# Optimization experiments

Hardware: AMD Instinct MI355X
Metric: run time of the kernel (lower is better)

The kernel has to match this reference:

```python
import jax, jax.numpy as jnp
import numpy as np

EPS = 1e-6


def setup_inputs() -> dict:
    key = jax.random.key(0)
    k1, k2, k3 = jax.random.split(key, 3)
    B, S, HC = 32, 16384, 4
    mixes = jax.random.normal(k1, (B, S, 2 * HC + HC * HC), dtype=jnp.float32)
    hc_scale = jax.random.uniform(k2, (3,), dtype=jnp.float32)
    hc_base = jax.random.normal(k3, (2 * HC + HC * HC,), dtype=jnp.float32)
    return {"mixes": mixes, "hc_scale": hc_scale, "hc_base": hc_base,
            "hc_mult": HC, "sinkhorn_iters": 20}


def reference(mixes, hc_scale, hc_base, hc_mult, sinkhorn_iters):
    hm = hc_mult
    pre = mixes[..., :hm]                       # [B,S,hm]
    post = mixes[..., hm:2 * hm]                # [B,S,hm]
    comb = mixes[..., 2 * hm:]                  # [B,S,hm*hm]
    comb = comb.reshape(comb.shape[:-1] + (hm, hm))  # [B,S,hm,hm]

    pre = jax.nn.sigmoid(pre * hc_scale[0] + hc_base[:hm]) + EPS
    post = 2.0 * jax.nn.sigmoid(post * hc_scale[1] + hc_base[hm:2 * hm])
    comb = comb * hc_scale[2] + hc_base[2 * hm:].reshape(hm, hm)
    comb = jax.nn.softmax(comb, axis=-1) + EPS

    # Sinkhorn normalization: alternate column / row normalization.
    comb = comb / (comb.sum(axis=-2, keepdims=True) + EPS)
    for _ in range(sinkhorn_iters - 1):
        comb = comb / (comb.sum(axis=-1, keepdims=True) + EPS)
        comb = comb / (comb.sum(axis=-2, keepdims=True) + EPS)
    return pre, post, comb
```

## Files before the change

### kernel.cpp

```cpp
#include <hip/hip_runtime.h>


constexpr float EPSF  = 1e-6f;
constexpr float LOG2E = 1.4426950408889634f;

__device__ __forceinline__ float frcp(float x) { return __builtin_amdgcn_rcpf(x); }
__device__ __forceinline__ float fexp(float x) { return __builtin_amdgcn_exp2f(x * LOG2E); }

__global__ __launch_bounds__(256) void hc_sinkhorn_kernel(
    const float* __restrict__ mixes,
    const float* __restrict__ hc_scale,
    const float* __restrict__ hc_base,
    float* __restrict__ out_pre,
    float* __restrict__ out_post,
    float* __restrict__ out_comb,
    int nrows)
{
    const int r = blockIdx.x * blockDim.x + threadIdx.x;
    if (r >= nrows) return;

    const float s0 = hc_scale[0];
    const float s1 = hc_scale[1];
    const float s2 = hc_scale[2];

    const float4* src = reinterpret_cast<const float4*>(mixes) + (size_t)r * 6;
    const float4 vpre  = src[0];
    const float4 vpost = src[1];
    const float4 c0    = src[2];
    const float4 c1    = src[3];
    const float4 c2    = src[4];
    const float4 c3    = src[5];

    float pre[4]  = {vpre.x,  vpre.y,  vpre.z,  vpre.w};
    float post[4] = {vpost.x, vpost.y, vpost.z, vpost.w};
    #pragma unroll
    for (int i = 0; i < 4; ++i) {
        pre[i]  = frcp(1.0f + fexp(-(pre[i]  * s0 + hc_base[i]))) + EPSF;
        post[i] = 2.0f * frcp(1.0f + fexp(-(post[i] * s1 + hc_base[4 + i])));
    }

    float c[4][4];
    c[0][0] = c0.x * s2 + hc_base[ 8]; c[0][1] = c0.y * s2 + hc_base[ 9];
    c[0][2] = c0.z * s2 + hc_base[10]; c[0][3] = c0.w * s2 + hc_base[11];
    c[1][0] = c1.x * s2 + hc_base[12]; c[1][1] = c1.y * s2 + hc_base[13];
    c[1][2] = c1.z * s2 + hc_base[14]; c[1][3] = c1.w * s2 + hc_base[15];
    c[2][0] = c2.x * s2 + hc_base[16]; c[2][1] = c2.y * s2 + hc_base[17];
    c[2][2] = c2.z * s2 + hc_base[18]; c[2][3] = c2.w * s2 + hc_base[19];
    c[3][0] = c3.x * s2 + hc_base[20]; c[3][1] = c3.y * s2 + hc_base[21];
    c[3][2] = c3.z * s2 + hc_base[22]; c[3][3] = c3.w * s2 + hc_base[23];

    #pragma unroll
    for (int i = 0; i < 4; ++i) {
        const float m  = fmaxf(fmaxf(c[i][0], c[i][1]), fmaxf(c[i][2], c[i][3]));
        const float e0 = fexp(c[i][0] - m);
        const float e1 = fexp(c[i][1] - m);
        const float e2 = fexp(c[i][2] - m);
        const float e3 = fexp(c[i][3] - m);
        const float rs = frcp(e0 + e1 + e2 + e3);
        c[i][0] = e0 * rs + EPSF;
        c[i][1] = e1 * rs + EPSF;
        c[i][2] = e2 * rs + EPSF;
        c[i][3] = e3 * rs + EPSF;
    }

    #pragma unroll
    for (int j = 0; j < 4; ++j) {
        const float s  = c[0][j] + c[1][j] + c[2][j] + c[3][j];
        const float rs = frcp(s + EPSF);
        c[0][j] *= rs; c[1][j] *= rs; c[2][j] *= rs; c[3][j] *= rs;
    }
    for (int it = 0; it < 19; ++it) {
        #pragma unroll
        for (int i = 0; i < 4; ++i) {
            const float s  = c[i][0] + c[i][1] + c[i][2] + c[i][3];
            const float rs = frcp(s + EPSF);
            c[i][0] *= rs; c[i][1] *= rs; c[i][2] *= rs; c[i][3] *= rs;
        }
        #pragma unroll
        for (int j = 0; j < 4; ++j) {
            const float s  = c[0][j] + c[1][j] + c[2][j] + c[3][j];
            const float rs = frcp(s + EPSF);
            c[0][j] *= rs; c[1][j] *= rs; c[2][j] *= rs; c[3][j] *= rs;
        }
    }

    reinterpret_cast<float4*>(out_pre)[r]  = make_float4(pre[0],  pre[1],  pre[2],  pre[3]);
    reinterpret_cast<float4*>(out_post)[r] = make_float4(post[0], post[1], post[2], post[3]);
    float4* oc = reinterpret_cast<float4*>(out_comb) + (size_t)r * 4;
    oc[0] = make_float4(c[0][0], c[0][1], c[0][2], c[0][3]);
    oc[1] = make_float4(c[1][0], c[1][1], c[1][2], c[1][3]);
    oc[2] = make_float4(c[2][0], c[2][1], c[2][2], c[2][3]);
    oc[3] = make_float4(c[3][0], c[3][1], c[3][2], c[3][3]);
}

extern "C" void kernel_launch(void* const* d_in, const int* in_sizes, int n_in,
                              void* d_out, int out_size, void* d_ws, size_t ws_size,
                              hipStream_t stream) {
    const float* mixes    = (const float*)d_in[0];
    const float* hc_scale = (const float*)d_in[1];
    const float* hc_base  = (const float*)d_in[2];

    const int nrows = in_sizes[0] / 24;
    float* out      = (float*)d_out;
    float* out_pre  = out;
    float* out_post = out + (size_t)nrows * 4;
    float* out_comb = out + (size_t)nrows * 8;

    const int block = 256;
    const int grid  = (nrows + block - 1) / block;
    hc_sinkhorn_kernel<<<grid, block, 0, stream>>>(
        mixes, hc_scale, hc_base, out_pre, out_post, out_comb, nrows);
}
```

Baseline: 113.4 us.

## Stage row loads and comb stores through padded LDS for coalesced access

```diff
diff --git a/kernel.cpp b/kernel.cpp
--- a/kernel.cpp
+++ b/kernel.cpp
@@ -4,50 +4,29 @@
 constexpr float EPSF  = 1e-6f;
 constexpr float LOG2E = 1.4426950408889634f;
 
+constexpr int RPB        = 256;
+constexpr int IN_STRIDE  = 25;
+constexpr int OUT_STRIDE = 17;
+
 __device__ __forceinline__ float frcp(float x) { return __builtin_amdgcn_rcpf(x); }
 __device__ __forceinline__ float fexp(float x) { return __builtin_amdgcn_exp2f(x * LOG2E); }
 
-__global__ __launch_bounds__(256) void hc_sinkhorn_kernel(
-    const float* __restrict__ mixes,
-    const float* __restrict__ hc_scale,
-    const float* __restrict__ hc_base,
-    float* __restrict__ out_pre,
-    float* __restrict__ out_post,
-    float* __restrict__ out_comb,
-    int nrows)
+__device__ __forceinline__ void compute_row(
+    const float row[24], const float base[24],
+    float s0, float s1, float s2,
+    float pre[4], float post[4], float c[4][4])
 {
-    const int r = blockIdx.x * blockDim.x + threadIdx.x;
-    if (r >= nrows) return;
-
-    const float s0 = hc_scale[0];
-    const float s1 = hc_scale[1];
-    const float s2 = hc_scale[2];
-
-    const float4* src = reinterpret_cast<const float4*>(mixes) + (size_t)r * 6;
-    const float4 vpre  = src[0];
-    const float4 vpost = src[1];
-    const float4 c0    = src[2];
-    const float4 c1    = src[3];
-    const float4 c2    = src[4];
-    const float4 c3    = src[5];
-
-    float pre[4]  = {vpre.x,  vpre.y,  vpre.z,  vpre.w};
-    float post[4] = {vpost.x, vpost.y, vpost.z, vpost.w};
     #pragma unroll
     for (int i = 0; i < 4; ++i) {
-        pre[i]  = frcp(1.0f + fexp(-(pre[i]  * s0 + hc_base[i]))) + EPSF;
-        post[i] = 2.0f * frcp(1.0f + fexp(-(post[i] * s1 + hc_base[4 + i])));
+        pre[i]  = frcp(1.0f + fexp(-(row[i]     * s0 + base[i])))     + EPSF;
+        post[i] = 2.0f * frcp(1.0f + fexp(-(row[4 + i] * s1 + base[4 + i])));
     }
 
-    float c[4][4];
-    c[0][0] = c0.x * s2 + hc_base[ 8]; c[0][1] = c0.y * s2 + hc_base[ 9];
-    c[0][2] = c0.z * s2 + hc_base[10]; c[0][3] = c0.w * s2 + hc_base[11];
-    c[1][0] = c1.x * s2 + hc_base[12]; c[1][1] = c1.y * s2 + hc_base[13];
-    c[1][2] = c1.z * s2 + hc_base[14]; c[1][3] = c1.w * s2 + hc_base[15];
-    c[2][0] = c2.x * s2 + hc_base[16]; c[2][1] = c2.y * s2 + hc_base[17];
-    c[2][2] = c2.z * s2 + hc_base[18]; c[2][3] = c2.w * s2 + hc_base[19];
-    c[3][0] = c3.x * s2 + hc_base[20]; c[3][1] = c3.y * s2 + hc_base[21];
-    c[3][2] = c3.z * s2 + hc_base[22]; c[3][3] = c3.w * s2 + hc_base[23];
+    #pragma unroll
+    for (int i = 0; i < 4; ++i)
+        #pragma unroll
+        for (int j = 0; j < 4; ++j)
+            c[i][j] = row[8 + 4 * i + j] * s2 + base[8 + 4 * i + j];
 
     #pragma unroll
     for (int i = 0; i < 4; ++i) {
@@ -65,32 +44,106 @@
 
     #pragma unroll
     for (int j = 0; j < 4; ++j) {
-        const float s  = c[0][j] + c[1][j] + c[2][j] + c[3][j];
-        const float rs = frcp(s + EPSF);
+        const float rs = frcp(c[0][j] + c[1][j] + c[2][j] + c[3][j] + EPSF);
         c[0][j] *= rs; c[1][j] *= rs; c[2][j] *= rs; c[3][j] *= rs;
     }
     for (int it = 0; it < 19; ++it) {
         #pragma unroll
         for (int i = 0; i < 4; ++i) {
-            const float s  = c[i][0] + c[i][1] + c[i][2] + c[i][3];
-            const float rs = frcp(s + EPSF);
+            const float rs = frcp(c[i][0] + c[i][1] + c[i][2] + c[i][3] + EPSF);
             c[i][0] *= rs; c[i][1] *= rs; c[i][2] *= rs; c[i][3] *= rs;
         }
         #pragma unroll
         for (int j = 0; j < 4; ++j) {
-            const float s  = c[0][j] + c[1][j] + c[2][j] + c[3][j];
-            const float rs = frcp(s + EPSF);
+            const float rs = frcp(c[0][j] + c[1][j] + c[2][j] + c[3][j] + EPSF);
             c[0][j] *= rs; c[1][j] *= rs; c[2][j] *= rs; c[3][j] *= rs;
         }
     }
+}
 
-    reinterpret_cast<float4*>(out_pre)[r]  = make_float4(pre[0],  pre[1],  pre[2],  pre[3]);
-    reinterpret_cast<float4*>(out_post)[r] = make_float4(post[0], post[1], post[2], post[3]);
-    float4* oc = reinterpret_cast<float4*>(out_comb) + (size_t)r * 4;
-    oc[0] = make_float4(c[0][0], c[0][1], c[0][2], c[0][3]);
-    oc[1] = make_float4(c[1][0], c[1][1], c[1][2], c[1][3]);
-    oc[2] = make_float4(c[2][0], c[2][1], c[2][2], c[2][3]);
-    oc[3] = make_float4(c[3][0], c[3][1], c[3][2], c[3][3]);
+__global__ __launch_bounds__(256) void hc_sinkhorn_kernel(
+    const float* __restrict__ mixes,
+    const float* __restrict__ hc_scale,
+    const float* __restrict__ hc_base,
+    float* __restrict__ out_pre,
+    float* __restrict__ out_post,
+    float* __restrict__ out_comb,
+    int nrows)
+{
+    __shared__ float lds[RPB * IN_STRIDE];
+
+    const int t       = threadIdx.x;
+    const int rowbase = blockIdx.x * RPB;
+
+    const float s0 = hc_scale[0];
+    const float s1 = hc_scale[1];
+    const float s2 = hc_scale[2];
+    float base[24];
+    #pragma unroll
+    for (int k = 0; k < 24; ++k) base[k] = hc_base[k];
+
+    if (rowbase + RPB <= nrows) {
+        const float4* src = reinterpret_cast<const float4*>(mixes) + (size_t)rowbase * 6;
+        #pragma unroll
+        for (int i = 0; i < 6; ++i) {
+            const int    g = i * 256 + t;
+            const float4 v = src[g];
+            const int    r = g / 6;
+            const int    j = g % 6;
+            float* dst = &lds[r * IN_STRIDE + j * 4];
+            dst[0] = v.x; dst[1] = v.y; dst[2] = v.z; dst[3] = v.w;
+        }
+        __syncthreads();
+
+        float row[24];
+        #pragma unroll
+        for (int k = 0; k < 24; ++k) row[k] = lds[t * IN_STRIDE + k];
+        __syncthreads();
+
+        float pre[4], post[4], c[4][4];
+        compute_row(row, base, s0, s1, s2, pre, post, c);
+
+        const int r = rowbase + t;
+        reinterpret_cast<float4*>(out_pre)[r]  = make_float4(pre[0],  pre[1],  pre[2],  pre[3]);
+        reinterpret_cast<float4*>(out_post)[r] = make_float4(post[0], post[1], post[2], post[3]);
+
+        #pragma unroll
+        for (int i = 0; i < 4; ++i)
+            #pragma unroll
+            for (int j = 0; j < 4; ++j)
+                lds[t * OUT_STRIDE + 4 * i + j] = c[i][j];
+        __syncthreads();
+
+        float4* dstc = reinterpret_cast<float4*>(out_comb) + (size_t)rowbase * 4;
+        #pragma unroll
+        for (int i = 0; i < 4; ++i) {
+            const int g  = i * 256 + t;
+            const int rr = g >> 2;
+            const int jj = g & 3;
+            const float* s = &lds[rr * OUT_STRIDE + 4 * jj];
+            dstc[g] = make_float4(s[0], s[1], s[2], s[3]);
+        }
+    } else {
+        const int r = rowbase + t;
+        if (r < nrows) {
+            const float4* src = reinterpret_cast<const float4*>(mixes) + (size_t)r * 6;
+            float row[24];
+            #pragma unroll
+            for (int i = 0; i < 6; ++i) {
+                const float4 v = src[i];
+                row[4 * i]     = v.x; row[4 * i + 1] = v.y;
+                row[4 * i + 2] = v.z; row[4 * i + 3] = v.w;
+            }
+            float pre[4], post[4], c[4][4];
+            compute_row(row, base, s0, s1, s2, pre, post, c);
+            reinterpret_cast<float4*>(out_pre)[r]  = make_float4(pre[0],  pre[1],  pre[2],  pre[3]);
+            reinterpret_cast<float4*>(out_post)[r] = make_float4(post[0], post[1], post[2], post[3]);
+            float4* oc = reinterpret_cast<float4*>(out_comb) + (size_t)r * 4;
+            #pragma unroll
+            for (int i = 0; i < 4; ++i)
+                oc[i] = make_float4(c[i][0], c[i][1], c[i][2], c[i][3]);
+        }
+    }
 }
 
 extern "C" void kernel_launch(void* const* d_in, const int* in_sizes, int n_in,
```

Result: no change. 112.9 us (-0.5%).
